# Kernel tuning notes

Measured on AMD Instinct MI355X. Metric: run time of the kernel, lower is better.

## Reference

```python
import jax, jax.numpy as jnp
import numpy as np

B, T, F_IN = 32768, 48, 8
OUT_STEPS = 12
TRAFFIC_COL = 4
# LSTM layer sizes: (in, hidden)
LAYERS = [(F_IN, 32), (32, 8), (8, 1), (1, 2), (2, 2), (2, 1)]


def _lstm(x, w_ih, w_hh, b):
    # x: [B, T, D], w_ih: [4H, D], w_hh: [4H, H], b: [4H] (b_ih + b_hh combined)
    Bn = x.shape[0]
    H = w_hh.shape[1]
    xg = jnp.einsum('btd,gd->btg', x, w_ih) + b  # [B, T, 4H] precomputed input gates

    def step(carry, xt):
        h, c = carry
        gates = xt + h @ w_hh.T  # [B, 4H]
        i, f, g, o = jnp.split(gates, 4, axis=-1)
        i = jax.nn.sigmoid(i)
        f = jax.nn.sigmoid(f)
        g = jnp.tanh(g)
        o = jax.nn.sigmoid(o)
        c = f * c + i * g
        h = o * jnp.tanh(c)
        return (h, c), h

    h0 = jnp.zeros((Bn, H), x.dtype)
    c0 = jnp.zeros((Bn, H), x.dtype)
    _, hs = jax.lax.scan(step, (h0, c0), jnp.swapaxes(xg, 0, 1))  # [T, B, H]
    return jnp.swapaxes(hs, 0, 1)


def setup_inputs() -> dict:
    key = jax.random.key(0)
    ks = iter(jax.random.split(key, 32))
    d = {'x': jax.random.normal(next(ks), (B, T, F_IN), jnp.float32)}
    names = ['e1', 'e2', 'e3', 'd1', 'd2', 'd3']
    for name, (din, h) in zip(names, LAYERS):
        s = 1.0 / np.sqrt(h)
        d[f'w_{name}_ih'] = jax.random.uniform(next(ks), (4 * h, din), jnp.float32, -s, s)
        d[f'w_{name}_hh'] = jax.random.uniform(next(ks), (4 * h, h), jnp.float32, -s, s)
        d[f'b_{name}'] = jax.random.uniform(next(ks), (4 * h,), jnp.float32, -s, s)
    d['fc1_w'] = jax.random.uniform(next(ks), (32, 60), jnp.float32, -1 / np.sqrt(60), 1 / np.sqrt(60))
    d['fc1_b'] = jax.random.uniform(next(ks), (32,), jnp.float32, -1 / np.sqrt(60), 1 / np.sqrt(60))
    d['fc2_w'] = jax.random.uniform(next(ks), (OUT_STEPS, 32), jnp.float32, -1 / np.sqrt(32), 1 / np.sqrt(32))
    d['fc2_b'] = jax.random.uniform(next(ks), (OUT_STEPS,), jnp.float32, -1 / np.sqrt(32), 1 / np.sqrt(32))
    return d


def reference(x,
              w_e1_ih, w_e1_hh, b_e1,
              w_e2_ih, w_e2_hh, b_e2,
              w_e3_ih, w_e3_hh, b_e3,
              w_d1_ih, w_d1_hh, b_d1,
              w_d2_ih, w_d2_hh, b_d2,
              w_d3_ih, w_d3_hh, b_d3,
              fc1_w, fc1_b, fc2_w, fc2_b):
    # Encoder: F_IN -> 32 -> 8 -> 1 (variational dropout disabled: eval mode)
    out = _lstm(x, w_e1_ih, w_e1_hh, b_e1)
    out = _lstm(out, w_e2_ih, w_e2_hh, b_e2)
    out = _lstm(out, w_e3_ih, w_e3_hh, b_e3)  # [B, T, 1]
    # Auxiliary traffic feature tail
    x_aux = x[:, -OUT_STEPS:, TRAFFIC_COL:TRAFFIC_COL + 1]  # [B, OUT_STEPS, 1]
    dec_in = jnp.concatenate([out, x_aux], axis=1)  # [B, 60, 1]
    # Decoder: 1 -> 2 -> 2 -> 1
    out = _lstm(dec_in, w_d1_ih, w_d1_hh, b_d1)
    out = _lstm(out, w_d2_ih, w_d2_hh, b_d2)
    out = _lstm(out, w_d3_ih, w_d3_hh, b_d3)  # [B, 60, 1]
    out = out.reshape(-1, 60)
    out = out @ fc1_w.T + fc1_b
    out = out @ fc2_w.T + fc2_b
    return out  # [B, OUT_STEPS]
```

## Files before the change

kernel.cpp:

```cpp
#include <hip/hip_runtime.h>
#include <cstddef>

#define TSEQ 48
#define TDEC 60

typedef float v2f __attribute__((ext_vector_type(2)));
typedef float v4f __attribute__((ext_vector_type(4)));

__device__ __forceinline__ float rcpf(float x){ return __builtin_amdgcn_rcpf(x); }
__device__ __forceinline__ float sigm(float x){ return rcpf(1.0f + __expf(-x)); }
__device__ __forceinline__ float tanhx(float x){ return 1.0f - 2.0f*rcpf(__expf(2.0f*x) + 1.0f); }

__device__ __forceinline__ v2f pkfma(v2f a, v2f b, v2f c){ return __builtin_elementwise_fma(a, b, c); }
#define SVLO(v) __builtin_shufflevector((v),(v),0,1)
#define SVHI(v) __builtin_shufflevector((v),(v),2,3)

__device__ __forceinline__ void load_pairs32(const float* p, v2f o[16]){
    #pragma unroll
    for (int q=0;q<8;++q){
        v4f v = *(const v4f*)(p + 4*q);
        o[2*q]   = SVLO(v);
        o[2*q+1] = SVHI(v);
    }
}

__global__ __launch_bounds__(256, 2)
void lstm_fused(const float* __restrict__ x,
                const float* __restrict__ w1i, const float* __restrict__ w1h, const float* __restrict__ b1,
                const float* __restrict__ w2i, const float* __restrict__ w2h, const float* __restrict__ b2,
                const float* __restrict__ w3i, const float* __restrict__ w3h, const float* __restrict__ b3,
                const float* __restrict__ w4i, const float* __restrict__ w4h, const float* __restrict__ b4,
                const float* __restrict__ w5i, const float* __restrict__ w5h, const float* __restrict__ b5,
                const float* __restrict__ w6i, const float* __restrict__ w6h, const float* __restrict__ b6,
                const float* __restrict__ fc1w, const float* __restrict__ fc1b,
                const float* __restrict__ fc2w, const float* __restrict__ fc2b,
                float* __restrict__ out)
{
    const int lane = threadIdx.x & 63;
    const int w    = threadIdx.x >> 6;
    const int g16  = lane >> 4;
    const int r16  = lane & 15;
    const int base = lane & 48;
    const int eb0  = w * 4;
    const int ebg  = eb0 + g16;
    const long gelem0 = (long)blockIdx.x * 16 + eb0;

    __shared__ float h1s[16][32];
    __shared__ float h2s[16][8];
    __shared__ float h6s[16][68];
    __shared__ float accs[16][36];

    #pragma unroll
    for (int e=0;e<4;++e){
        if (lane<32) h1s[eb0+e][lane]=0.f;
        if (lane<8)  h2s[eb0+e][lane]=0.f;
    }

    const int  u1  = lane >> 1;
    const int  rA  = ((lane & 1) << 5) + u1;
    const int  rB  = 64 + rA;
    const bool evn = (lane & 1) == 0;
    v2f w1iA2[4], w1iB2[4], w1hA2[16], w1hB2[16];
    {
        #pragma unroll
        for (int q=0;q<2;++q){
            v4f va = *(const v4f*)(w1i + rA*8 + 4*q);
            v4f vb = *(const v4f*)(w1i + rB*8 + 4*q);
            w1iA2[2*q]=SVLO(va); w1iA2[2*q+1]=SVHI(va);
            w1iB2[2*q]=SVLO(vb); w1iB2[2*q+1]=SVHI(vb);
        }
        load_pairs32(w1h + rA*32, w1hA2);
        load_pairs32(w1h + rB*32, w1hB2);
    }
    const float bA_ = b1[rA], bB_ = b1[rB];

    const int r2 = lane & 31;
    v2f w2i2[16], w2h2[4];
    {
        load_pairs32(w2i + r2*32, w2i2);
        v4f v0 = *(const v4f*)(w2h + r2*8);
        v4f v1 = *(const v4f*)(w2h + r2*8 + 4);
        w2h2[0]=SVLO(v0); w2h2[1]=SVHI(v0); w2h2[2]=SVLO(v1); w2h2[3]=SVHI(v1);
    }
    const float b2_ = b2[r2];
    const bool tg2 = ((r2>>3)==2);

    const int r34 = r16 & 3;
    float w3i_[8];
    {
        const float4* p = (const float4*)(w3i + r34*8);
        float4 v0=p[0], v1=p[1];
        w3i_[0]=v0.x;w3i_[1]=v0.y;w3i_[2]=v0.z;w3i_[3]=v0.w;
        w3i_[4]=v1.x;w3i_[5]=v1.y;w3i_[6]=v1.z;w3i_[7]=v1.w;
    }
    const float w3h_ = w3h[r34], b3_ = b3[r34];
    const bool tg3 = (r34==2);

    const int r8 = lane & 7;
    const float w4i_ = w4i[r8], w4h0 = w4h[r8*2], w4h1 = w4h[r8*2+1], b4_ = b4[r8];
    const float w5i0 = w5i[r8*2], w5i1 = w5i[r8*2+1], w5h0 = w5h[r8*2], w5h1 = w5h[r8*2+1], b5_ = b5[r8];
    const bool tg45 = ((r8>>1)==2);
    const float w6i0 = w6i[r34*2], w6i1 = w6i[r34*2+1], w6h_ = w6h[r34], b6_ = b6[r34];

    float c1e[4] = {0.f,0.f,0.f,0.f};
    float c2p[2] = {0.f,0.f};
    float c3=0.f, h3=0.f;
    float c4=0.f, h4a=0.f, h4b=0.f;
    float c5=0.f, h5a=0.f, h5b=0.f;
    float c6=0.f, h6=0.f;

    for (int t=0; t<TDEC; ++t){
        float din;
        if (t < TSEQ){
            #pragma unroll
            for (int e=0;e<4;++e){
                const float* xr = x + (size_t)(gelem0+e)*(TSEQ*8) + t*8;
                v4f xa = *(const v4f*)xr;
                v4f xb = *(const v4f*)(xr+4);
                v2f xp[4] = { SVLO(xa), SVHI(xa), SVLO(xb), SVHI(xb) };
                v2f h1p[16];
                load_pairs32(&h1s[eb0+e][0], h1p);

                v2f aq[2] = { (v2f){bA_,0.f}, (v2f){0.f,0.f} };
                v2f bq[2] = { (v2f){bB_,0.f}, (v2f){0.f,0.f} };
                #pragma unroll
                for (int j=0;j<4;++j){
                    aq[j&1] = pkfma(w1iA2[j], xp[j], aq[j&1]);
                    bq[j&1] = pkfma(w1iB2[j], xp[j], bq[j&1]);
                }
                #pragma unroll
                for (int k=0;k<16;++k){
                    aq[k&1] = pkfma(w1hA2[k], h1p[k], aq[k&1]);
                    bq[k&1] = pkfma(w1hB2[k], h1p[k], bq[k&1]);
                }
                const v2f as = aq[0] + aq[1];
                const v2f bs = bq[0] + bq[1];
                const float gA = as[0] + as[1];
                const float gB = bs[0] + bs[1];

                const float actA = sigm(gA);
                const float sB   = sigm(evn ? 2.f*gB : gB);
                const float actB = evn ? 2.f*sB-1.f : sB;
                const float pA = __shfl_xor(actA, 1);
                const float pB = __shfl_xor(actB, 1);
                const float iv = evn ? actA : pA;
                const float fv = evn ? pA   : actA;
                const float gv = evn ? actB : pB;
                const float ov = evn ? pB   : actB;
                c1e[e] = fv*c1e[e] + iv*gv;
                const float h1n = ov*tanhx(c1e[e]);
                if (evn) h1s[eb0+e][u1] = h1n;
            }

            #pragma unroll
            for (int p=0;p<2;++p){
                const int eb2 = eb0 + p*2 + (lane>>5);
                v2f h1p[16];
                load_pairs32(&h1s[eb2][0], h1p);
                v2f h2p[4];
                {
                    v4f v0 = *(const v4f*)&h2s[eb2][0];
                    v4f v1 = *(const v4f*)&h2s[eb2][4];
                    h2p[0]=SVLO(v0); h2p[1]=SVHI(v0); h2p[2]=SVLO(v1); h2p[3]=SVHI(v1);
                }
                v2f qq[2] = { (v2f){b2_,0.f}, (v2f){0.f,0.f} };
                #pragma unroll
                for (int k=0;k<16;++k) qq[k&1] = pkfma(w2i2[k], h1p[k], qq[k&1]);
                #pragma unroll
                for (int k=0;k<4;++k)  qq[k&1] = pkfma(w2h2[k], h2p[k], qq[k&1]);
                const v2f qs = qq[0] + qq[1];
                const float g2 = qs[0] + qs[1];

                const float s2 = sigm(tg2 ? 2.f*g2 : g2);
                const float a2 = tg2 ? 2.f*s2-1.f : s2;
                const float f2  = __shfl_xor(a2, 8);
                const float gv2 = __shfl_xor(a2, 16);
                const float o2  = __shfl_xor(a2, 24);
                c2p[p] = f2*c2p[p] + a2*gv2;
                const float h2n = o2*tanhx(c2p[p]);
                if (r2<8) h2s[eb2][r2] = h2n;
            }

            float h2g[8];
            {
                float4 v0 = *reinterpret_cast<float4*>(&h2s[ebg][0]);
                float4 v1 = *reinterpret_cast<float4*>(&h2s[ebg][4]);
                h2g[0]=v0.x;h2g[1]=v0.y;h2g[2]=v0.z;h2g[3]=v0.w;
                h2g[4]=v1.x;h2g[5]=v1.y;h2g[6]=v1.z;h2g[7]=v1.w;
            }
            float g3 = b3_ + w3h_*h3;
            #pragma unroll
            for (int j=0;j<8;++j) g3 += w3i_[j]*h2g[j];
            const float s3 = sigm(tg3 ? 2.f*g3 : g3);
            const float a3 = tg3 ? 2.f*s3-1.f : s3;
            const float e1x = __shfl_xor(a3, 1);
            const float e2x = __shfl_xor(a3, 2);
            const float e3x = __shfl_xor(a3, 3);
            c3 = e1x*c3 + a3*e2x;
            h3 = __shfl(e3x*tanhx(c3), base);
            din = h3;
        } else {
            din = x[(size_t)(gelem0+g16)*(TSEQ*8) + (t-12)*8 + 4];
        }

        {
            const float g = b4_ + w4i_*din + w4h0*h4a + w4h1*h4b;
            const float s = sigm(tg45 ? 2.f*g : g);
            const float a = tg45 ? 2.f*s-1.f : s;
            const float y2 = __shfl_xor(a, 2);
            const float y4 = __shfl_xor(a, 4);
            const float y6 = __shfl_xor(a, 6);
            c4 = y2*c4 + a*y4;
            const float hl = y6*tanhx(c4);
            h4a = __shfl(hl, base);
            h4b = __shfl(hl, base+1);
        }
        {
            const float g = b5_ + w5i0*h4a + w5i1*h4b + w5h0*h5a + w5h1*h5b;
            const float s = sigm(tg45 ? 2.f*g : g);
            const float a = tg45 ? 2.f*s-1.f : s;
            const float y2 = __shfl_xor(a, 2);
            const float y4 = __shfl_xor(a, 4);
            const float y6 = __shfl_xor(a, 6);
            c5 = y2*c5 + a*y4;
            const float hl = y6*tanhx(c5);
            h5a = __shfl(hl, base);
            h5b = __shfl(hl, base+1);
        }
        {
            const float g = b6_ + w6i0*h5a + w6i1*h5b + w6h_*h6;
            const float s = sigm(tg3 ? 2.f*g : g);
            const float a = tg3 ? 2.f*s-1.f : s;
            const float z1 = __shfl_xor(a, 1);
            const float z2 = __shfl_xor(a, 2);
            const float z3 = __shfl_xor(a, 3);
            c6 = z1*c6 + a*z2;
            h6 = __shfl(z3*tanhx(c6), base);
        }
        if (r16==0) h6s[ebg][t] = h6;
    }

    {
        float a0 = fc1b[r16], a1 = fc1b[16+r16];
        const float* f0 = fc1w + r16*60;
        const float* f1 = fc1w + (16+r16)*60;
        #pragma unroll
        for (int q=0;q<15;++q){
            float4 hv = *reinterpret_cast<float4*>(&h6s[ebg][4*q]);
            float4 u0 = *reinterpret_cast<const float4*>(f0 + 4*q);
            float4 u1v= *reinterpret_cast<const float4*>(f1 + 4*q);
            a0 += u0.x*hv.x + u0.y*hv.y + u0.z*hv.z + u0.w*hv.w;
            a1 += u1v.x*hv.x + u1v.y*hv.y + u1v.z*hv.z + u1v.w*hv.w;
        }
        accs[ebg][r16]    = a0;
        accs[ebg][16+r16] = a1;
    }
    if (r16 < 12){
        float o = fc2b[r16];
        const float* fr = fc2w + r16*32;
        #pragma unroll
        for (int q=0;q<8;++q){
            float4 av = *reinterpret_cast<float4*>(&accs[ebg][4*q]);
            float4 wv = *reinterpret_cast<const float4*>(fr + 4*q);
            o += wv.x*av.x + wv.y*av.y + wv.z*av.z + wv.w*av.w;
        }
        out[(size_t)(gelem0+g16)*12 + r16] = o;
    }
}

extern "C" void kernel_launch(void* const* d_in, const int* in_sizes, int n_in,
                              void* d_out, int out_size, void* d_ws, size_t ws_size,
                              hipStream_t stream)
{
    const float* x    = (const float*)d_in[0];
    const float* w1i  = (const float*)d_in[1];
    const float* w1h  = (const float*)d_in[2];
    const float* b1   = (const float*)d_in[3];
    const float* w2i  = (const float*)d_in[4];
    const float* w2h  = (const float*)d_in[5];
    const float* b2   = (const float*)d_in[6];
    const float* w3i  = (const float*)d_in[7];
    const float* w3h  = (const float*)d_in[8];
    const float* b3   = (const float*)d_in[9];
    const float* w4i  = (const float*)d_in[10];
    const float* w4h  = (const float*)d_in[11];
    const float* b4   = (const float*)d_in[12];
    const float* w5i  = (const float*)d_in[13];
    const float* w5h  = (const float*)d_in[14];
    const float* b5   = (const float*)d_in[15];
    const float* w6i  = (const float*)d_in[16];
    const float* w6h  = (const float*)d_in[17];
    const float* b6   = (const float*)d_in[18];
    const float* fc1w = (const float*)d_in[19];
    const float* fc1b = (const float*)d_in[20];
    const float* fc2w = (const float*)d_in[21];
    const float* fc2b = (const float*)d_in[22];

    lstm_fused<<<dim3(32768/16), dim3(256), 0, stream>>>(
        x, w1i,w1h,b1, w2i,w2h,b2, w3i,w3h,b3,
        w4i,w4h,b4, w5i,w5h,b5, w6i,w6h,b6,
        fc1w,fc1b, fc2w,fc2b, (float*)d_out);
}
```

Before: 701.7 us.

## Process eight sequences per wavefront and split encoder/decoder time loops

Each wavefront now handles 8 batch elements instead of 4, halving the grid to 1024 blocks. The small layers 3-6 are remapped from 16-lane to 8-lane groups so all 64 lanes do useful work, where they previously ran at low lane utilisation. The time loop is split into an encoder-length loop and a separate decoder-tail loop, which removes the per-step branch. The trade-off is more serial layer-1/2 work per wave, more per-thread state, and possibly lower occupancy from the larger shared memory and register use.

```diff
diff --git a/kernel.cpp b/kernel.cpp
--- a/kernel.cpp
+++ b/kernel.cpp
@@ -36,22 +36,24 @@
                 const float* __restrict__ fc2w, const float* __restrict__ fc2b,
                 float* __restrict__ out)
 {
-    const int lane = threadIdx.x & 63;
-    const int w    = threadIdx.x >> 6;
-    const int g16  = lane >> 4;
-    const int r16  = lane & 15;
-    const int base = lane & 48;
-    const int eb0  = w * 4;
-    const int ebg  = eb0 + g16;
-    const long gelem0 = (long)blockIdx.x * 16 + eb0;
-
-    __shared__ float h1s[16][32];
-    __shared__ float h2s[16][8];
-    __shared__ float h6s[16][68];
-    __shared__ float accs[16][36];
+    const int lane  = threadIdx.x & 63;
+    const int w     = threadIdx.x >> 6;
+    const int g8    = lane >> 3;
+    const int r8    = lane & 7;
+    const int base8 = lane & 56;
+    const int g16   = lane >> 4;
+    const int r16   = lane & 15;
+    const int eb0   = w * 8;
+    const int ebg8  = eb0 + g8;
+    const long gelem0 = (long)blockIdx.x * 32 + eb0;
+
+    __shared__ float h1s[32][32];
+    __shared__ float h2s[32][8];
+    __shared__ float h6s[32][68];
+    __shared__ float accs[32][36];
 
     #pragma unroll
-    for (int e=0;e<4;++e){
+    for (int e=0;e<8;++e){
         if (lane<32) h1s[eb0+e][lane]=0.f;
         if (lane<8)  h2s[eb0+e][lane]=0.f;
     }
@@ -85,7 +87,7 @@
     const float b2_ = b2[r2];
     const bool tg2 = ((r2>>3)==2);
 
-    const int r34 = r16 & 3;
+    const int r34 = r8 & 3;
     float w3i_[8];
     {
         const float4* p = (const float4*)(w3i + r34*8);
@@ -96,112 +98,106 @@
     const float w3h_ = w3h[r34], b3_ = b3[r34];
     const bool tg3 = (r34==2);
 
-    const int r8 = lane & 7;
     const float w4i_ = w4i[r8], w4h0 = w4h[r8*2], w4h1 = w4h[r8*2+1], b4_ = b4[r8];
     const float w5i0 = w5i[r8*2], w5i1 = w5i[r8*2+1], w5h0 = w5h[r8*2], w5h1 = w5h[r8*2+1], b5_ = b5[r8];
     const bool tg45 = ((r8>>1)==2);
     const float w6i0 = w6i[r34*2], w6i1 = w6i[r34*2+1], w6h_ = w6h[r34], b6_ = b6[r34];
 
-    float c1e[4] = {0.f,0.f,0.f,0.f};
-    float c2p[2] = {0.f,0.f};
+    float c1e[8] = {0.f,0.f,0.f,0.f,0.f,0.f,0.f,0.f};
+    float c2p[4] = {0.f,0.f,0.f,0.f};
     float c3=0.f, h3=0.f;
     float c4=0.f, h4a=0.f, h4b=0.f;
     float c5=0.f, h5a=0.f, h5b=0.f;
     float c6=0.f, h6=0.f;
 
-    for (int t=0; t<TDEC; ++t){
-        float din;
-        if (t < TSEQ){
-            #pragma unroll
-            for (int e=0;e<4;++e){
-                const float* xr = x + (size_t)(gelem0+e)*(TSEQ*8) + t*8;
-                v4f xa = *(const v4f*)xr;
-                v4f xb = *(const v4f*)(xr+4);
-                v2f xp[4] = { SVLO(xa), SVHI(xa), SVLO(xb), SVHI(xb) };
-                v2f h1p[16];
-                load_pairs32(&h1s[eb0+e][0], h1p);
-
-                v2f aq[2] = { (v2f){bA_,0.f}, (v2f){0.f,0.f} };
-                v2f bq[2] = { (v2f){bB_,0.f}, (v2f){0.f,0.f} };
-                #pragma unroll
-                for (int j=0;j<4;++j){
-                    aq[j&1] = pkfma(w1iA2[j], xp[j], aq[j&1]);
-                    bq[j&1] = pkfma(w1iB2[j], xp[j], bq[j&1]);
-                }
-                #pragma unroll
-                for (int k=0;k<16;++k){
-                    aq[k&1] = pkfma(w1hA2[k], h1p[k], aq[k&1]);
-                    bq[k&1] = pkfma(w1hB2[k], h1p[k], bq[k&1]);
-                }
-                const v2f as = aq[0] + aq[1];
-                const v2f bs = bq[0] + bq[1];
-                const float gA = as[0] + as[1];
-                const float gB = bs[0] + bs[1];
-
-                const float actA = sigm(gA);
-                const float sB   = sigm(evn ? 2.f*gB : gB);
-                const float actB = evn ? 2.f*sB-1.f : sB;
-                const float pA = __shfl_xor(actA, 1);
-                const float pB = __shfl_xor(actB, 1);
-                const float iv = evn ? actA : pA;
-                const float fv = evn ? pA   : actA;
-                const float gv = evn ? actB : pB;
-                const float ov = evn ? pB   : actB;
-                c1e[e] = fv*c1e[e] + iv*gv;
-                const float h1n = ov*tanhx(c1e[e]);
-                if (evn) h1s[eb0+e][u1] = h1n;
-            }
-
-            #pragma unroll
-            for (int p=0;p<2;++p){
-                const int eb2 = eb0 + p*2 + (lane>>5);
-                v2f h1p[16];
-                load_pairs32(&h1s[eb2][0], h1p);
-                v2f h2p[4];
-                {
-                    v4f v0 = *(const v4f*)&h2s[eb2][0];
-                    v4f v1 = *(const v4f*)&h2s[eb2][4];
-                    h2p[0]=SVLO(v0); h2p[1]=SVHI(v0); h2p[2]=SVLO(v1); h2p[3]=SVHI(v1);
-                }
-                v2f qq[2] = { (v2f){b2_,0.f}, (v2f){0.f,0.f} };
-                #pragma unroll
-                for (int k=0;k<16;++k) qq[k&1] = pkfma(w2i2[k], h1p[k], qq[k&1]);
-                #pragma unroll
-                for (int k=0;k<4;++k)  qq[k&1] = pkfma(w2h2[k], h2p[k], qq[k&1]);
-                const v2f qs = qq[0] + qq[1];
-                const float g2 = qs[0] + qs[1];
-
-                const float s2 = sigm(tg2 ? 2.f*g2 : g2);
-                const float a2 = tg2 ? 2.f*s2-1.f : s2;
-                const float f2  = __shfl_xor(a2, 8);
-                const float gv2 = __shfl_xor(a2, 16);
-                const float o2  = __shfl_xor(a2, 24);
-                c2p[p] = f2*c2p[p] + a2*gv2;
-                const float h2n = o2*tanhx(c2p[p]);
-                if (r2<8) h2s[eb2][r2] = h2n;
-            }
-
-            float h2g[8];
+    for (int t=0; t<TSEQ; ++t){
+        #pragma unroll
+        for (int e=0;e<8;++e){
+            const float* xr = x + (size_t)(gelem0+e)*(TSEQ*8) + t*8;
+            v4f xa = *(const v4f*)xr;
+            v4f xb = *(const v4f*)(xr+4);
+            v2f xp[4] = { SVLO(xa), SVHI(xa), SVLO(xb), SVHI(xb) };
+            v2f h1p[16];
+            load_pairs32(&h1s[eb0+e][0], h1p);
+
+            v2f aq[2] = { (v2f){bA_,0.f}, (v2f){0.f,0.f} };
+            v2f bq[2] = { (v2f){bB_,0.f}, (v2f){0.f,0.f} };
+            #pragma unroll
+            for (int j=0;j<4;++j){
+                aq[j&1] = pkfma(w1iA2[j], xp[j], aq[j&1]);
+                bq[j&1] = pkfma(w1iB2[j], xp[j], bq[j&1]);
+            }
+            #pragma unroll
+            for (int k=0;k<16;++k){
+                aq[k&1] = pkfma(w1hA2[k], h1p[k], aq[k&1]);
+                bq[k&1] = pkfma(w1hB2[k], h1p[k], bq[k&1]);
+            }
+            const v2f as = aq[0] + aq[1];
+            const v2f bs = bq[0] + bq[1];
+            const float gA = as[0] + as[1];
+            const float gB = bs[0] + bs[1];
+
+            const float actA = sigm(gA);
+            const float sB   = sigm(evn ? 2.f*gB : gB);
+            const float actB = evn ? 2.f*sB-1.f : sB;
+            const float pA = __shfl_xor(actA, 1);
+            const float pB = __shfl_xor(actB, 1);
+            const float iv = evn ? actA : pA;
+            const float fv = evn ? pA   : actA;
+            const float gv = evn ? actB : pB;
+            const float ov = evn ? pB   : actB;
+            c1e[e] = fv*c1e[e] + iv*gv;
+            const float h1n = ov*tanhx(c1e[e]);
+            if (evn) h1s[eb0+e][u1] = h1n;
+        }
+
+        #pragma unroll
+        for (int p=0;p<4;++p){
+            const int eb2 = eb0 + p*2 + (lane>>5);
+            v2f h1p[16];
+            load_pairs32(&h1s[eb2][0], h1p);
+            v2f h2p[4];
             {
-                float4 v0 = *reinterpret_cast<float4*>(&h2s[ebg][0]);
-                float4 v1 = *reinterpret_cast<float4*>(&h2s[ebg][4]);
-                h2g[0]=v0.x;h2g[1]=v0.y;h2g[2]=v0.z;h2g[3]=v0.w;
-                h2g[4]=v1.x;h2g[5]=v1.y;h2g[6]=v1.z;h2g[7]=v1.w;
-            }
-            float g3 = b3_ + w3h_*h3;
-            #pragma unroll
-            for (int j=0;j<8;++j) g3 += w3i_[j]*h2g[j];
-            const float s3 = sigm(tg3 ? 2.f*g3 : g3);
-            const float a3 = tg3 ? 2.f*s3-1.f : s3;
-            const float e1x = __shfl_xor(a3, 1);
-            const float e2x = __shfl_xor(a3, 2);
-            const float e3x = __shfl_xor(a3, 3);
-            c3 = e1x*c3 + a3*e2x;
-            h3 = __shfl(e3x*tanhx(c3), base);
-            din = h3;
-        } else {
-            din = x[(size_t)(gelem0+g16)*(TSEQ*8) + (t-12)*8 + 4];
-        }
+                v4f v0 = *(const v4f*)&h2s[eb2][0];
+                v4f v1 = *(const v4f*)&h2s[eb2][4];
+                h2p[0]=SVLO(v0); h2p[1]=SVHI(v0); h2p[2]=SVLO(v1); h2p[3]=SVHI(v1);
+            }
+            v2f qq[2] = { (v2f){b2_,0.f}, (v2f){0.f,0.f} };
+            #pragma unroll
+            for (int k=0;k<16;++k) qq[k&1] = pkfma(w2i2[k], h1p[k], qq[k&1]);
+            #pragma unroll
+            for (int k=0;k<4;++k)  qq[k&1] = pkfma(w2h2[k], h2p[k], qq[k&1]);
+            const v2f qs = qq[0] + qq[1];
+            const float g2 = qs[0] + qs[1];
+
+            const float s2 = sigm(tg2 ? 2.f*g2 : g2);
+            const float a2 = tg2 ? 2.f*s2-1.f : s2;
+            const float f2  = __shfl_xor(a2, 8);
+            const float gv2 = __shfl_xor(a2, 16);
+            const float o2  = __shfl_xor(a2, 24);
+            c2p[p] = f2*c2p[p] + a2*gv2;
+            const float h2n = o2*tanhx(c2p[p]);
+            if (r2<8) h2s[eb2][r2] = h2n;
+        }
+
+        float h2g[8];
+        {
+            v4f v0 = *(const v4f*)&h2s[ebg8][0];
+            v4f v1 = *(const v4f*)&h2s[ebg8][4];
+            h2g[0]=v0[0];h2g[1]=v0[1];h2g[2]=v0[2];h2g[3]=v0[3];
+            h2g[4]=v1[0];h2g[5]=v1[1];h2g[6]=v1[2];h2g[7]=v1[3];
+        }
+        float g3 = b3_ + w3h_*h3;
+        #pragma unroll
+        for (int j=0;j<8;++j) g3 += w3i_[j]*h2g[j];
+        const float s3 = sigm(tg3 ? 2.f*g3 : g3);
+        const float a3 = tg3 ? 2.f*s3-1.f : s3;
+        const float e1x = __shfl_xor(a3, 1);
+        const float e2x = __shfl_xor(a3, 2);
+        const float e3x = __shfl_xor(a3, 3);
+        c3 = e1x*c3 + a3*e2x;
+        h3 = __shfl(e3x*tanhx(c3), base8);
+        const float din = h3;
 
         {
             const float g = b4_ + w4i_*din + w4h0*h4a + w4h1*h4b;
@@ -212,8 +208,8 @@
             const float y6 = __shfl_xor(a, 6);
             c4 = y2*c4 + a*y4;
             const float hl = y6*tanhx(c4);
-            h4a = __shfl(hl, base);
-            h4b = __shfl(hl, base+1);
+            h4a = __shfl(hl, base8);
+            h4b = __shfl(hl, base8+1);
         }
         {
             const float g = b5_ + w5i0*h4a + w5i1*h4b + w5h0*h5a + w5h1*h5b;
@@ -224,8 +220,8 @@
             const float y6 = __shfl_xor(a, 6);
             c5 = y2*c5 + a*y4;
             const float hl = y6*tanhx(c5);
-            h5a = __shfl(hl, base);
-            h5b = __shfl(hl, base+1);
+            h5a = __shfl(hl, base8);
+            h5b = __shfl(hl, base8+1);
         }
         {
             const float g = b6_ + w6i0*h5a + w6i1*h5b + w6h_*h6;
@@ -235,36 +231,79 @@
             const float z2 = __shfl_xor(a, 2);
             const float z3 = __shfl_xor(a, 3);
             c6 = z1*c6 + a*z2;
-            h6 = __shfl(z3*tanhx(c6), base);
-        }
-        if (r16==0) h6s[ebg][t] = h6;
-    }
-
-    {
-        float a0 = fc1b[r16], a1 = fc1b[16+r16];
-        const float* f0 = fc1w + r16*60;
-        const float* f1 = fc1w + (16+r16)*60;
-        #pragma unroll
-        for (int q=0;q<15;++q){
-            float4 hv = *reinterpret_cast<float4*>(&h6s[ebg][4*q]);
-            float4 u0 = *reinterpret_cast<const float4*>(f0 + 4*q);
-            float4 u1v= *reinterpret_cast<const float4*>(f1 + 4*q);
-            a0 += u0.x*hv.x + u0.y*hv.y + u0.z*hv.z + u0.w*hv.w;
-            a1 += u1v.x*hv.x + u1v.y*hv.y + u1v.z*hv.z + u1v.w*hv.w;
-        }
-        accs[ebg][r16]    = a0;
-        accs[ebg][16+r16] = a1;
-    }
-    if (r16 < 12){
-        float o = fc2b[r16];
-        const float* fr = fc2w + r16*32;
-        #pragma unroll
-        for (int q=0;q<8;++q){
-            float4 av = *reinterpret_cast<float4*>(&accs[ebg][4*q]);
-            float4 wv = *reinterpret_cast<const float4*>(fr + 4*q);
-            o += wv.x*av.x + wv.y*av.y + wv.z*av.z + wv.w*av.w;
-        }
-        out[(size_t)(gelem0+g16)*12 + r16] = o;
+            h6 = __shfl(z3*tanhx(c6), base8);
+        }
+        if (r8==0) h6s[ebg8][t] = h6;
+    }
+
+    for (int t=TSEQ; t<TDEC; ++t){
+        const float din = x[(size_t)(gelem0+g8)*(TSEQ*8) + (t-12)*8 + 4];
+        {
+            const float g = b4_ + w4i_*din + w4h0*h4a + w4h1*h4b;
+            const float s = sigm(tg45 ? 2.f*g : g);
+            const float a = tg45 ? 2.f*s-1.f : s;
+            const float y2 = __shfl_xor(a, 2);
+            const float y4 = __shfl_xor(a, 4);
+            const float y6 = __shfl_xor(a, 6);
+            c4 = y2*c4 + a*y4;
+            const float hl = y6*tanhx(c4);
+            h4a = __shfl(hl, base8);
+            h4b = __shfl(hl, base8+1);
+        }
+        {
+            const float g = b5_ + w5i0*h4a + w5i1*h4b + w5h0*h5a + w5h1*h5b;
+            const float s = sigm(tg45 ? 2.f*g : g);
+            const float a = tg45 ? 2.f*s-1.f : s;
+            const float y2 = __shfl_xor(a, 2);
+            const float y4 = __shfl_xor(a, 4);
+            const float y6 = __shfl_xor(a, 6);
+            c5 = y2*c5 + a*y4;
+            const float hl = y6*tanhx(c5);
+            h5a = __shfl(hl, base8);
+            h5b = __shfl(hl, base8+1);
+        }
+        {
+            const float g = b6_ + w6i0*h5a + w6i1*h5b + w6h_*h6;
+            const float s = sigm(tg3 ? 2.f*g : g);
+            const float a = tg3 ? 2.f*s-1.f : s;
+            const float z1 = __shfl_xor(a, 1);
+            const float z2 = __shfl_xor(a, 2);
+            const float z3 = __shfl_xor(a, 3);
+            c6 = z1*c6 + a*z2;
+            h6 = __shfl(z3*tanhx(c6), base8);
+        }
+        if (r8==0) h6s[ebg8][t] = h6;
+    }
+
+    #pragma unroll
+    for (int p=0;p<2;++p){
+        const int ebgE = eb0 + p*4 + g16;
+        {
+            float a0 = fc1b[r16], a1 = fc1b[16+r16];
+            const float* f0 = fc1w + r16*60;
+            const float* f1 = fc1w + (16+r16)*60;
+            #pragma unroll
+            for (int q=0;q<15;++q){
+                float4 hv = *reinterpret_cast<float4*>(&h6s[ebgE][4*q]);
+                float4 u0 = *reinterpret_cast<const float4*>(f0 + 4*q);
+                float4 u1v= *reinterpret_cast<const float4*>(f1 + 4*q);
+                a0 += u0.x*hv.x + u0.y*hv.y + u0.z*hv.z + u0.w*hv.w;
+                a1 += u1v.x*hv.x + u1v.y*hv.y + u1v.z*hv.z + u1v.w*hv.w;
+            }
+            accs[ebgE][r16]    = a0;
+            accs[ebgE][16+r16] = a1;
+        }
+        if (r16 < 12){
+            float o = fc2b[r16];
+            const float* fr = fc2w + r16*32;
+            #pragma unroll
+            for (int q=0;q<8;++q){
+                float4 av = *reinterpret_cast<float4*>(&accs[ebgE][4*q]);
+                float4 wv = *reinterpret_cast<const float4*>(fr + 4*q);
+                o += wv.x*av.x + wv.y*av.y + wv.z*av.z + wv.w*av.w;
+            }
+            out[(size_t)(gelem0 + p*4 + g16)*12 + r16] = o;
+        }
     }
 }
 
@@ -296,7 +335,7 @@
     const float* fc2w = (const float*)d_in[21];
     const float* fc2b = (const float*)d_in[22];
 
-    lstm_fused<<<dim3(32768/16), dim3(256), 0, stream>>>(
+    lstm_fused<<<dim3(32768/32), dim3(256), 0, stream>>>(
         x, w1i,w1h,b1, w2i,w2h,b2, w3i,w3h,b3,
         w4i,w4h,b4, w5i,w5h,b5, w6i,w6h,b6,
         fc1w,fc1b, fc2w,fc2b, (float*)d_out);
```

Measured after the change: 621.4 us. 1.13x faster.
